# Kernel tuning notes

Measured on AMD Instinct MI355X. Metric: run time of the kernel, lower is better.

The kernel has to match this reference:

```python
import jax, jax.numpy as jnp
import numpy as np

B, S, HID = 4, 1024, 1024
NH, HD = 16, 64  # num heads, head dim


def setup_inputs() -> dict:
    key = jax.random.key(0)
    ks = jax.random.split(key, 8)
    scale = 0.02
    return {
        "hidden_states": jax.random.normal(ks[0], (B, S, HID), dtype=jnp.float32),
        "attention_mask": jnp.ones((B, 1, 1, S), dtype=jnp.float32),
        "Wq": jax.random.normal(ks[1], (HID, HID), dtype=jnp.float32) * scale,
        "bq": jnp.zeros((HID,), dtype=jnp.float32),
        "Wk": jax.random.normal(ks[2], (HID, HID), dtype=jnp.float32) * scale,
        "bk": jnp.zeros((HID,), dtype=jnp.float32),
        "Wv": jax.random.normal(ks[3], (HID, HID), dtype=jnp.float32) * scale,
        "bv": jnp.zeros((HID,), dtype=jnp.float32),
    }


def reference(hidden_states, attention_mask, Wq, bq, Wk, bk, Wv, bv):
    # Linear projections: torch nn.Linear computes x @ W.T + b
    q = hidden_states @ Wq.T + bq  # [B,S,HID]
    k = hidden_states @ Wk.T + bk
    v = hidden_states @ Wv.T + bv

    def split_heads(x):
        return x.reshape(B, S, NH, HD).transpose(0, 2, 1, 3)  # [B,NH,S,HD]

    q, k, v = split_heads(q), split_heads(k), split_heads(v)

    scores = jnp.einsum("bhqd,bhkd->bhqk", q, k) / jnp.sqrt(jnp.float32(HD))
    # faithful to original: scores - (2 - mask) * 1e6
    scores = scores - (2.0 - attention_mask) * 1.0e6
    probs = jax.nn.softmax(scores, axis=-1)
    # dropout: eval mode -> identity
    ctx = jnp.einsum("bhqk,bhkd->bhqd", probs, v)  # [B,NH,S,HD]
    ctx = ctx.transpose(0, 2, 1, 3).reshape(B, S, HID)
    return ctx
```

## Files before the change

### kernel.cpp

```cpp
#include <hip/hip_runtime.h>
#include <math.h>

#define B_ 4
#define S_ 1024
#define HID_ 1024
#define NH_ 16
#define HD_ 64
#define NTOK (B_ * S_)

typedef __attribute__((ext_vector_type(4))) float f32x4;
typedef __attribute__((ext_vector_type(8))) short bf16x8;

__device__ __forceinline__ unsigned short f2bf(float f) {
    union { float f; unsigned int u; } v; v.f = f;
    unsigned int r = v.u + 0x7fffu + ((v.u >> 16) & 1u);
    return (unsigned short)(r >> 16);
}
__device__ __forceinline__ float bf2f(unsigned short u) {
    return __uint_as_float((unsigned int)u << 16);
}

__device__ __forceinline__ void load_lds16(const void* g, void* l) {
    __builtin_amdgcn_global_load_lds(
        (const __attribute__((address_space(1))) unsigned int*)(uintptr_t)g,
        (__attribute__((address_space(3))) unsigned int*)(uintptr_t)l,
        16, 0, 0);
}

__global__ __launch_bounds__(256) void cvt_all(
    const float* __restrict__ x, const float* __restrict__ wq,
    const float* __restrict__ wk, const float* __restrict__ wv,
    unsigned short* __restrict__ xb, unsigned short* __restrict__ wqb,
    unsigned short* __restrict__ wkb, unsigned short* __restrict__ wvb)
{
    const int which = blockIdx.y;
    const float* src = which == 0 ? x : which == 1 ? wq : which == 2 ? wk : wv;
    unsigned short* dst = which == 0 ? xb : which == 1 ? wqb : which == 2 ? wkb : wvb;
    const int n4 = (which == 0) ? (NTOK * HID_ / 4) : (HID_ * HID_ / 4);
    int i = blockIdx.x * 256 + threadIdx.x;
    if (i < n4) {
        float4 f = ((const float4*)src)[i];
        ushort4 o = make_ushort4(f2bf(f.x), f2bf(f.y), f2bf(f.z), f2bf(f.w));
        ((ushort4*)dst)[i] = o;
    }
}

__global__ __launch_bounds__(256) void qkv_gemm_mfma(
    const unsigned short* __restrict__ xb,
    const unsigned short* __restrict__ Wqb, const float* __restrict__ bq,
    const unsigned short* __restrict__ Wkb, const float* __restrict__ bk,
    const unsigned short* __restrict__ Wvb, const float* __restrict__ bv,
    unsigned short* __restrict__ qout, unsigned short* __restrict__ kout,
    unsigned short* __restrict__ vtout)
{
    const int which = blockIdx.z;
    const unsigned short* __restrict__ W = which == 0 ? Wqb : which == 1 ? Wkb : Wvb;
    const float* __restrict__ bias       = which == 0 ? bq  : which == 1 ? bk  : bv;

    __shared__ unsigned short As[128 * 32];
    __shared__ unsigned short Bs[128 * 32];

    const int t    = threadIdx.x;
    const int lane = t & 63;
    const int w    = t >> 6;
    const int wr   = w >> 1;
    const int wc   = w & 1;

    const int bm = blockIdx.x;
    const int bn = blockIdx.y;

    const int srow = t >> 2;
    const int sk   = (t & 3) << 3;
    const unsigned short* gA = xb + (size_t)(bm * 128 + srow) * HID_ + sk;
    const unsigned short* gB = W  + (size_t)(bn * 128 + srow) * HID_ + sk;

    const f32x4 zero = {0.f, 0.f, 0.f, 0.f};
    f32x4 acc[4][4];
    #pragma unroll
    for (int i = 0; i < 4; ++i)
        #pragma unroll
        for (int j = 0; j < 4; ++j) acc[i][j] = zero;

    const int lrow = lane & 15;
    const int lk   = (lane >> 4) << 3;

    for (int k0 = 0; k0 < HID_; k0 += 32) {
        __syncthreads();
        load_lds16(gA + k0,              (char*)As + t * 16);
        load_lds16(gA + 64 * HID_ + k0,  (char*)As + 4096 + t * 16);
        load_lds16(gB + k0,              (char*)Bs + t * 16);
        load_lds16(gB + 64 * HID_ + k0,  (char*)Bs + 4096 + t * 16);
        __syncthreads();

        bf16x8 af[4], bf[4];
        #pragma unroll
        for (int i = 0; i < 4; ++i)
            af[i] = *(const bf16x8*)&As[(wr * 64 + i * 16 + lrow) * 32 + lk];
        #pragma unroll
        for (int j = 0; j < 4; ++j)
            bf[j] = *(const bf16x8*)&Bs[(wc * 64 + j * 16 + lrow) * 32 + lk];
        #pragma unroll
        for (int i = 0; i < 4; ++i)
            #pragma unroll
            for (int j = 0; j < 4; ++j)
                acc[i][j] = __builtin_amdgcn_mfma_f32_16x16x32_bf16(
                    af[i], bf[j], acc[i][j], 0, 0, 0);
    }

    const int col   = lane & 15;
    const int rbase = (lane >> 4) << 2;
    #pragma unroll
    for (int j = 0; j < 4; ++j) {
        const int feat = bn * 128 + wc * 64 + j * 16 + col;
        const int h = feat >> 6, d = feat & 63;
        const float bias_v = bias[feat];
        #pragma unroll
        for (int i = 0; i < 4; ++i) {
            const int tok0 = bm * 128 + wr * 64 + i * 16 + rbase;
            #pragma unroll
            for (int r = 0; r < 4; ++r) {
                const int tok = tok0 + r;
                const int b = tok >> 10, s = tok & 1023;
                const float val = acc[i][j][r] + bias_v;
                if (which == 2) {
                    vtout[((size_t)((b << 4) + h) << 16) + ((size_t)d << 10) + s] = f2bf(val);
                } else {
                    const size_t off = ((size_t)((b << 4) + h) << 16) + ((size_t)s << 6) + d;
                    if (which == 0) qout[off] = f2bf(val);
                    else            kout[off] = f2bf(val);
                }
            }
        }
    }
}

__global__ __launch_bounds__(256) void attn_mfma(
    const unsigned short* __restrict__ Q, const unsigned short* __restrict__ K,
    const unsigned short* __restrict__ Vt, const float* __restrict__ mask,
    float* __restrict__ out)
{
    __shared__ unsigned short Qs[128 * 64];
    __shared__ unsigned short Ks[64 * 64];
    __shared__ unsigned short Vts[64 * 64];
    __shared__ unsigned short Ps[4][32 * 72];
    __shared__ float Ms[64];

    const int t    = threadIdx.x;
    const int lane = t & 63;
    const int w    = t >> 6;
    const int g    = lane >> 4;
    const int ln   = lane & 15;

    const int bh = blockIdx.x;
    const int b  = bh >> 4;
    const int h  = bh & 15;
    const int q0 = blockIdx.y << 7;

    const unsigned short* __restrict__ qg = Q  + ((size_t)bh << 16);
    const unsigned short* __restrict__ kg = K  + ((size_t)bh << 16);
    const unsigned short* __restrict__ vg = Vt + ((size_t)bh << 16);

    #pragma unroll
    for (int i = 0; i < 4; ++i) {
        const int G   = i * 256 + t;
        const int row = G >> 3;
        const int c   = (G & 7) ^ (row & 7);
        load_lds16(qg + (size_t)(q0 + row) * 64 + c * 8, (char*)Qs + i * 4096 + t * 16);
    }

    const f32x4 zero = {0.f, 0.f, 0.f, 0.f};
    f32x4 O[2][4];
    #pragma unroll
    for (int i = 0; i < 2; ++i)
        #pragma unroll
        for (int j = 0; j < 4; ++j) O[i][j] = zero;
    float lacc[2][4] = {};

    for (int kt = 0; kt < 16; ++kt) {
        const int kt0 = kt << 6;
        __syncthreads();
        #pragma unroll
        for (int i = 0; i < 2; ++i) {
            const int G   = i * 256 + t;
            const int row = G >> 3;
            const int c   = (G & 7) ^ (row & 7);
            load_lds16(kg + (size_t)(kt0 + row) * 64 + c * 8,   (char*)Ks  + i * 4096 + t * 16);
            load_lds16(vg + (size_t)row * 1024 + kt0 + c * 8,   (char*)Vts + i * 4096 + t * 16);
        }
        if (t < 64) Ms[t] = mask[(b << 10) + kt0 + t];
        __syncthreads();

        f32x4 sacc[2][4];
        #pragma unroll
        for (int i = 0; i < 2; ++i)
            #pragma unroll
            for (int j = 0; j < 4; ++j) sacc[i][j] = zero;
        #pragma unroll
        for (int ks = 0; ks < 2; ++ks) {
            bf16x8 af[2], bfj[4];
            #pragma unroll
            for (int i = 0; i < 2; ++i) {
                const int row = w * 32 + i * 16 + ln;
                af[i] = *(const bf16x8*)&Qs[row * 64 + (((ks * 4 + g) ^ (row & 7)) << 3)];
            }
            #pragma unroll
            for (int j = 0; j < 4; ++j) {
                const int row = j * 16 + ln;
                bfj[j] = *(const bf16x8*)&Ks[row * 64 + (((ks * 4 + g) ^ (row & 7)) << 3)];
            }
            #pragma unroll
            for (int i = 0; i < 2; ++i)
                #pragma unroll
                for (int j = 0; j < 4; ++j)
                    sacc[i][j] = __builtin_amdgcn_mfma_f32_16x16x32_bf16(
                        af[i], bfj[j], sacc[i][j], 0, 0, 0);
        }

        float mv[4];
        #pragma unroll
        for (int j = 0; j < 4; ++j) mv[j] = (2.0f - Ms[j * 16 + ln]) * 1.0e6f;

        #pragma unroll
        for (int i = 0; i < 2; ++i)
            #pragma unroll
            for (int j = 0; j < 4; ++j)
                #pragma unroll
                for (int r = 0; r < 4; ++r) {
                    const float sv = sacc[i][j][r] * 0.125f - mv[j];
                    const float p  = __expf(sv + 1.0e6f);
                    const unsigned short pb = f2bf(p);
                    Ps[w][(i * 16 + g * 4 + r) * 72 + j * 16 + ln] = pb;
                    lacc[i][r] += bf2f(pb);
                }
        asm volatile("s_waitcnt lgkmcnt(0)" ::: "memory");

        #pragma unroll
        for (int ks = 0; ks < 2; ++ks) {
            bf16x8 pf[2], vf[4];
            #pragma unroll
            for (int i = 0; i < 2; ++i)
                pf[i] = *(const bf16x8*)&Ps[w][(i * 16 + ln) * 72 + ks * 32 + g * 8];
            #pragma unroll
            for (int j = 0; j < 4; ++j) {
                const int row = j * 16 + ln;
                vf[j] = *(const bf16x8*)&Vts[row * 64 + (((ks * 4 + g) ^ (row & 7)) << 3)];
            }
            #pragma unroll
            for (int i = 0; i < 2; ++i)
                #pragma unroll
                for (int j = 0; j < 4; ++j)
                    O[i][j] = __builtin_amdgcn_mfma_f32_16x16x32_bf16(
                        pf[i], vf[j], O[i][j], 0, 0, 0);
        }
    }

    #pragma unroll
    for (int i = 0; i < 2; ++i) {
        #pragma unroll
        for (int r = 0; r < 4; ++r) {
            float rs = lacc[i][r];
            rs += __shfl_xor(rs, 1);
            rs += __shfl_xor(rs, 2);
            rs += __shfl_xor(rs, 4);
            rs += __shfl_xor(rs, 8);
            const float inv = 1.0f / rs;
            const int q = q0 + w * 32 + i * 16 + g * 4 + r;
            const size_t base = (((size_t)(b << 10) + q) << 10) + (h << 6);
            #pragma unroll
            for (int j = 0; j < 4; ++j)
                out[base + j * 16 + ln] = O[i][j][r] * inv;
        }
    }
}

extern "C" void kernel_launch(void* const* d_in, const int* in_sizes, int n_in,
                              void* d_out, int out_size, void* d_ws, size_t ws_size,
                              hipStream_t stream) {
    const float* hs   = (const float*)d_in[0];
    const float* mask = (const float*)d_in[1];
    const float* Wq   = (const float*)d_in[2];
    const float* bq   = (const float*)d_in[3];
    const float* Wk   = (const float*)d_in[4];
    const float* bk   = (const float*)d_in[5];
    const float* Wv   = (const float*)d_in[6];
    const float* bv   = (const float*)d_in[7];
    float* out = (float*)d_out;

    char* ws = (char*)d_ws;
    unsigned short* xb  = (unsigned short*)(ws);
    unsigned short* wqb = (unsigned short*)(ws + ((size_t)8  << 20));
    unsigned short* wkb = (unsigned short*)(ws + ((size_t)10 << 20));
    unsigned short* wvb = (unsigned short*)(ws + ((size_t)12 << 20));
    unsigned short* qb  = (unsigned short*)(ws + ((size_t)14 << 20));
    unsigned short* kb  = (unsigned short*)(ws + ((size_t)22 << 20));
    unsigned short* vtb = (unsigned short*)(ws + ((size_t)30 << 20));

    cvt_all<<<dim3(4096, 4), 256, 0, stream>>>(hs, Wq, Wk, Wv, xb, wqb, wkb, wvb);
    qkv_gemm_mfma<<<dim3(NTOK / 128, HID_ / 128, 3), 256, 0, stream>>>(
        xb, wqb, bq, wkb, bk, wvb, bv, qb, kb, vtb);
    attn_mfma<<<dim3(B_ * NH_, S_ / 128), 256, 0, stream>>>(qb, kb, vtb, mask, out);
}
```

Baseline: 165.0 us.

## Swap GEMM operands for V-transpose stores and shrink attention query tile

For the V projection, the GEMM operands are swapped so the accumulator layout puts consecutive tokens across lanes. The transposed V stores then become contiguous along the sequence dimension instead of strided. The attention kernel halves its query tile to 64 rows (16 per wave), doubling the grid for better CU occupancy. It computes S^T = K·Q so each lane owns one query column, writes P with packed 64-bit LDS stores, and reduces row sums through a small LDS table. Each block now reloads K/V per 64 queries, doubling K/V global traffic, and per-wave MFMA reuse drops.

```diff
diff --git a/kernel.cpp b/kernel.cpp
--- a/kernel.cpp
+++ b/kernel.cpp
@@ -69,10 +69,15 @@
     const int bm = blockIdx.x;
     const int bn = blockIdx.y;
 
+    const unsigned short* __restrict__ Arow = (which == 2) ? W  : xb;
+    const unsigned short* __restrict__ Brow = (which == 2) ? xb : W;
+    const int am0 = (which == 2) ? bn * 128 : bm * 128;
+    const int bn0 = (which == 2) ? bm * 128 : bn * 128;
+
     const int srow = t >> 2;
     const int sk   = (t & 3) << 3;
-    const unsigned short* gA = xb + (size_t)(bm * 128 + srow) * HID_ + sk;
-    const unsigned short* gB = W  + (size_t)(bn * 128 + srow) * HID_ + sk;
+    const unsigned short* gA = Arow + (size_t)(am0 + srow) * HID_ + sk;
+    const unsigned short* gB = Brow + (size_t)(bn0 + srow) * HID_ + sk;
 
     const f32x4 zero = {0.f, 0.f, 0.f, 0.f};
     f32x4 acc[4][4];
@@ -109,23 +114,38 @@
 
     const int col   = lane & 15;
     const int rbase = (lane >> 4) << 2;
-    #pragma unroll
-    for (int j = 0; j < 4; ++j) {
-        const int feat = bn * 128 + wc * 64 + j * 16 + col;
-        const int h = feat >> 6, d = feat & 63;
-        const float bias_v = bias[feat];
+    if (which == 2) {
         #pragma unroll
         for (int i = 0; i < 4; ++i) {
-            const int tok0 = bm * 128 + wr * 64 + i * 16 + rbase;
             #pragma unroll
             for (int r = 0; r < 4; ++r) {
-                const int tok = tok0 + r;
-                const int b = tok >> 10, s = tok & 1023;
-                const float val = acc[i][j][r] + bias_v;
-                if (which == 2) {
-                    vtout[((size_t)((b << 4) + h) << 16) + ((size_t)d << 10) + s] = f2bf(val);
-                } else {
+                const int feat = bn * 128 + wr * 64 + i * 16 + rbase + r;
+                const int h = feat >> 6, d = feat & 63;
+                const float bias_v = bias[feat];
+                #pragma unroll
+                for (int j = 0; j < 4; ++j) {
+                    const int tok = bm * 128 + wc * 64 + j * 16 + col;
+                    const int b = tok >> 10, s = tok & 1023;
+                    vtout[((size_t)((b << 4) + h) << 16) + ((size_t)d << 10) + s] =
+                        f2bf(acc[i][j][r] + bias_v);
+                }
+            }
+        }
+    } else {
+        #pragma unroll
+        for (int j = 0; j < 4; ++j) {
+            const int feat = bn * 128 + wc * 64 + j * 16 + col;
+            const int h = feat >> 6, d = feat & 63;
+            const float bias_v = bias[feat];
+            #pragma unroll
+            for (int i = 0; i < 4; ++i) {
+                const int tok0 = bm * 128 + wr * 64 + i * 16 + rbase;
+                #pragma unroll
+                for (int r = 0; r < 4; ++r) {
+                    const int tok = tok0 + r;
+                    const int b = tok >> 10, s = tok & 1023;
                     const size_t off = ((size_t)((b << 4) + h) << 16) + ((size_t)s << 6) + d;
+                    const float val = acc[i][j][r] + bias_v;
                     if (which == 0) qout[off] = f2bf(val);
                     else            kout[off] = f2bf(val);
                 }
@@ -139,10 +159,11 @@
     const unsigned short* __restrict__ Vt, const float* __restrict__ mask,
     float* __restrict__ out)
 {
-    __shared__ unsigned short Qs[128 * 64];
+    __shared__ unsigned short Qs[64 * 64];
     __shared__ unsigned short Ks[64 * 64];
     __shared__ unsigned short Vts[64 * 64];
-    __shared__ unsigned short Ps[4][32 * 72];
+    __shared__ unsigned short Ps[4][16 * 72];
+    __shared__ float Ls[4][16];
     __shared__ float Ms[64];
 
     const int t    = threadIdx.x;
@@ -154,14 +175,14 @@
     const int bh = blockIdx.x;
     const int b  = bh >> 4;
     const int h  = bh & 15;
-    const int q0 = blockIdx.y << 7;
+    const int q0 = blockIdx.y << 6;
 
     const unsigned short* __restrict__ qg = Q  + ((size_t)bh << 16);
     const unsigned short* __restrict__ kg = K  + ((size_t)bh << 16);
     const unsigned short* __restrict__ vg = Vt + ((size_t)bh << 16);
 
     #pragma unroll
-    for (int i = 0; i < 4; ++i) {
+    for (int i = 0; i < 2; ++i) {
         const int G   = i * 256 + t;
         const int row = G >> 3;
         const int c   = (G & 7) ^ (row & 7);
@@ -169,12 +190,12 @@
     }
 
     const f32x4 zero = {0.f, 0.f, 0.f, 0.f};
-    f32x4 O[2][4];
+    f32x4 O[4];
     #pragma unroll
-    for (int i = 0; i < 2; ++i)
-        #pragma unroll
-        for (int j = 0; j < 4; ++j) O[i][j] = zero;
-    float lacc[2][4] = {};
+    for (int j = 0; j < 4; ++j) O[j] = zero;
+    float lacc = 0.f;
+
+    const int qrow = w * 16 + ln;
 
     for (int kt = 0; kt < 16; ++kt) {
         const int kt0 = kt << 6;
@@ -184,92 +205,76 @@
             const int G   = i * 256 + t;
             const int row = G >> 3;
             const int c   = (G & 7) ^ (row & 7);
-            load_lds16(kg + (size_t)(kt0 + row) * 64 + c * 8,   (char*)Ks  + i * 4096 + t * 16);
-            load_lds16(vg + (size_t)row * 1024 + kt0 + c * 8,   (char*)Vts + i * 4096 + t * 16);
+            load_lds16(kg + (size_t)(kt0 + row) * 64 + c * 8, (char*)Ks  + i * 4096 + t * 16);
+            load_lds16(vg + (size_t)row * 1024 + kt0 + c * 8, (char*)Vts + i * 4096 + t * 16);
         }
         if (t < 64) Ms[t] = mask[(b << 10) + kt0 + t];
         __syncthreads();
 
-        f32x4 sacc[2][4];
-        #pragma unroll
-        for (int i = 0; i < 2; ++i)
-            #pragma unroll
-            for (int j = 0; j < 4; ++j) sacc[i][j] = zero;
+        f32x4 sacc[4];
+        #pragma unroll
+        for (int j = 0; j < 4; ++j) sacc[j] = zero;
         #pragma unroll
         for (int ks = 0; ks < 2; ++ks) {
-            bf16x8 af[2], bfj[4];
-            #pragma unroll
-            for (int i = 0; i < 2; ++i) {
-                const int row = w * 32 + i * 16 + ln;
-                af[i] = *(const bf16x8*)&Qs[row * 64 + (((ks * 4 + g) ^ (row & 7)) << 3)];
-            }
+            bf16x8 qf = *(const bf16x8*)&Qs[qrow * 64 + (((ks * 4 + g) ^ (qrow & 7)) << 3)];
+            bf16x8 kf[4];
             #pragma unroll
             for (int j = 0; j < 4; ++j) {
-                const int row = j * 16 + ln;
-                bfj[j] = *(const bf16x8*)&Ks[row * 64 + (((ks * 4 + g) ^ (row & 7)) << 3)];
-            }
-            #pragma unroll
-            for (int i = 0; i < 2; ++i)
-                #pragma unroll
-                for (int j = 0; j < 4; ++j)
-                    sacc[i][j] = __builtin_amdgcn_mfma_f32_16x16x32_bf16(
-                        af[i], bfj[j], sacc[i][j], 0, 0, 0);
-        }
-
-        float mv[4];
-        #pragma unroll
-        for (int j = 0; j < 4; ++j) mv[j] = (2.0f - Ms[j * 16 + ln]) * 1.0e6f;
-
-        #pragma unroll
-        for (int i = 0; i < 2; ++i)
+                const int krow = j * 16 + ln;
+                kf[j] = *(const bf16x8*)&Ks[krow * 64 + (((ks * 4 + g) ^ (krow & 7)) << 3)];
+            }
             #pragma unroll
             for (int j = 0; j < 4; ++j)
-                #pragma unroll
-                for (int r = 0; r < 4; ++r) {
-                    const float sv = sacc[i][j][r] * 0.125f - mv[j];
-                    const float p  = __expf(sv + 1.0e6f);
-                    const unsigned short pb = f2bf(p);
-                    Ps[w][(i * 16 + g * 4 + r) * 72 + j * 16 + ln] = pb;
-                    lacc[i][r] += bf2f(pb);
-                }
+                sacc[j] = __builtin_amdgcn_mfma_f32_16x16x32_bf16(
+                    kf[j], qf, sacc[j], 0, 0, 0);
+        }
+
+        #pragma unroll
+        for (int j = 0; j < 4; ++j) {
+            unsigned short pb[4];
+            #pragma unroll
+            for (int r = 0; r < 4; ++r) {
+                const int key = j * 16 + g * 4 + r;
+                const float sv = sacc[j][r] * 0.125f - (2.0f - Ms[key]) * 1.0e6f;
+                pb[r] = f2bf(__expf(sv + 1.0e6f));
+                lacc += bf2f(pb[r]);
+            }
+            uint2 pk;
+            pk.x = (unsigned int)pb[0] | ((unsigned int)pb[1] << 16);
+            pk.y = (unsigned int)pb[2] | ((unsigned int)pb[3] << 16);
+            *(uint2*)&Ps[w][ln * 72 + j * 16 + (g << 2)] = pk;
+        }
         asm volatile("s_waitcnt lgkmcnt(0)" ::: "memory");
 
         #pragma unroll
         for (int ks = 0; ks < 2; ++ks) {
-            bf16x8 pf[2], vf[4];
-            #pragma unroll
-            for (int i = 0; i < 2; ++i)
-                pf[i] = *(const bf16x8*)&Ps[w][(i * 16 + ln) * 72 + ks * 32 + g * 8];
+            bf16x8 pf = *(const bf16x8*)&Ps[w][ln * 72 + ks * 32 + (g << 3)];
+            bf16x8 vf[4];
             #pragma unroll
             for (int j = 0; j < 4; ++j) {
-                const int row = j * 16 + ln;
-                vf[j] = *(const bf16x8*)&Vts[row * 64 + (((ks * 4 + g) ^ (row & 7)) << 3)];
-            }
-            #pragma unroll
-            for (int i = 0; i < 2; ++i)
-                #pragma unroll
-                for (int j = 0; j < 4; ++j)
-                    O[i][j] = __builtin_amdgcn_mfma_f32_16x16x32_bf16(
-                        pf[i], vf[j], O[i][j], 0, 0, 0);
-        }
-    }
-
+                const int vrow = j * 16 + ln;
+                vf[j] = *(const bf16x8*)&Vts[vrow * 64 + (((ks * 4 + g) ^ (vrow & 7)) << 3)];
+            }
+            #pragma unroll
+            for (int j = 0; j < 4; ++j)
+                O[j] = __builtin_amdgcn_mfma_f32_16x16x32_bf16(
+                    pf, vf[j], O[j], 0, 0, 0);
+        }
+    }
+
+    float rs = lacc;
+    rs += __shfl_xor(rs, 16);
+    rs += __shfl_xor(rs, 32);
+    if (lane < 16) Ls[w][ln] = rs;
+    asm volatile("s_waitcnt lgkmcnt(0)" ::: "memory");
     #pragma unroll
-    for (int i = 0; i < 2; ++i) {
-        #pragma unroll
-        for (int r = 0; r < 4; ++r) {
-            float rs = lacc[i][r];
-            rs += __shfl_xor(rs, 1);
-            rs += __shfl_xor(rs, 2);
-            rs += __shfl_xor(rs, 4);
-            rs += __shfl_xor(rs, 8);
-            const float inv = 1.0f / rs;
-            const int q = q0 + w * 32 + i * 16 + g * 4 + r;
-            const size_t base = (((size_t)(b << 10) + q) << 10) + (h << 6);
-            #pragma unroll
-            for (int j = 0; j < 4; ++j)
-                out[base + j * 16 + ln] = O[i][j][r] * inv;
-        }
+    for (int r = 0; r < 4; ++r) {
+        const float inv = 1.0f / Ls[w][(g << 2) + r];
+        const int q = q0 + w * 16 + (g << 2) + r;
+        const size_t base = (((size_t)(b << 10) + q) << 10) + (h << 6);
+        #pragma unroll
+        for (int j = 0; j < 4; ++j)
+            out[base + j * 16 + ln] = O[j][r] * inv;
     }
 }
 
@@ -298,5 +303,5 @@
     cvt_all<<<dim3(4096, 4), 256, 0, stream>>>(hs, Wq, Wk, Wv, xb, wqb, wkb, wvb);
     qkv_gemm_mfma<<<dim3(NTOK / 128, HID_ / 128, 3), 256, 0, stream>>>(
         xb, wqb, bq, wkb, bk, wvb, bv, qb, kb, vtb);
-    attn_mfma<<<dim3(B_ * NH_, S_ / 128), 256, 0, stream>>>(qb, kb, vtb, mask, out);
-}
+    attn_mfma<<<dim3(B_ * NH_, S_ / 64), 256, 0, stream>>>(qb, kb, vtb, mask, out);
+}
```

Measured after the change: 171.4 us. +3.9%, slower.
